# Kernel tuning notes

Hardware: AMD Instinct MI355X
Metric: run time of the kernel (lower is better)

Reference implementation:

```python
import jax, jax.numpy as jnp
import numpy as np

B, N0, D, H = 64, 512, 512, 2048  # graphs, nodes/graph, d_hidden, mlp hidden


def _mlp(x, W1, b1, W2, b2, W3, b3):
    h = jax.nn.relu(x @ W1 + b1)
    h = jax.nn.relu(h @ W2 + b2)
    return h @ W3 + b3


def setup_inputs() -> dict:
    key = jax.random.key(0)
    ks = jax.random.split(key, 16)
    total = B * N0
    x = jax.random.normal(ks[0], (total, D), jnp.float32)
    node_type = jax.random.randint(ks[1], (total,), 0, 4, jnp.int32)
    action_mask = jax.random.bernoulli(ks[2], 0.5, (total,))
    node_indices = jnp.tile(jnp.arange(N0, dtype=jnp.int32), B)
    batch = jnp.repeat(jnp.arange(B, dtype=jnp.int32), N0)
    N = jnp.full((B,), N0, dtype=jnp.int32)

    def lin(k, fan_in, fan_out):
        kw, kb = jax.random.split(k)
        bound = 1.0 / np.sqrt(fan_in)
        W = jax.random.uniform(kw, (fan_in, fan_out), jnp.float32, -bound, bound)
        b = jax.random.uniform(kb, (fan_out,), jnp.float32, -bound, bound)
        return W, b

    mlp_W1, mlp_b1 = lin(ks[3], D, H)
    mlp_W2, mlp_b2 = lin(ks[4], H, H)
    mlp_W3, mlp_b3 = lin(ks[5], H, 1)
    vf_W1, vf_b1 = lin(ks[6], D, H)
    vf_W2, vf_b2 = lin(ks[7], H, H)
    vf_W3, vf_b3 = lin(ks[8], H, 1)
    return dict(x=x, node_type=node_type, action_mask=action_mask,
                node_indices=node_indices, batch=batch, N=N,
                mlp_W1=mlp_W1, mlp_b1=mlp_b1, mlp_W2=mlp_W2, mlp_b2=mlp_b2,
                mlp_W3=mlp_W3, mlp_b3=mlp_b3,
                vf_W1=vf_W1, vf_b1=vf_b1, vf_W2=vf_W2, vf_b2=vf_b2,
                vf_W3=vf_W3, vf_b3=vf_b3)


def reference(x, node_type, action_mask, node_indices, batch, N,
              mlp_W1, mlp_b1, mlp_W2, mlp_b2, mlp_W3, mlp_b3,
              vf_W1, vf_b1, vf_W2, vf_b2, vf_W3, vf_b3):
    nb = N.shape[0]
    # global mean pool over graphs
    counts = jax.ops.segment_sum(jnp.ones((x.shape[0],), x.dtype), batch, num_segments=nb)
    h_mean = jax.ops.segment_sum(x, batch, num_segments=nb) / counts[:, None]
    # masked gather -> MLP -> scatter with -inf fill, expressed as masked select
    z_node = _mlp(x, mlp_W1, mlp_b1, mlp_W2, mlp_b2, mlp_W3, mlp_b3)[:, 0]
    z_all = jnp.where(action_mask, z_node, -jnp.inf)
    z = z_all.reshape(nb, -1)  # multi_length=False: all graphs have N[0] nodes
    v = _mlp(h_mean, vf_W1, vf_b1, vf_W2, vf_b2, vf_W3, vf_b3)
    return z, v
```

## Files before the change

### kernel.cpp

```cpp
#include <hip/hip_runtime.h>
#include <cstdint>
#include <cmath>


typedef __bf16 bf16_t;
typedef float  f32x4  __attribute__((ext_vector_type(4)));
typedef int    i32x4  __attribute__((ext_vector_type(4)));
typedef int    i32x8  __attribute__((ext_vector_type(8)));

#define NB      64
#define N0      512
#define DIM     512
#define HID     2048
#define TOTAL   32768
#define ZNEG    -3.0e38f

__device__ __forceinline__ void gload16(const void* g, void* l) {
  __builtin_amdgcn_global_load_lds(
      (const uint32_t __attribute__((address_space(1)))*)g,
      (uint32_t __attribute__((address_space(3)))*)l, 16, 0, 0);
}

__device__ __forceinline__ unsigned char to_fp8(float f) {
  return (unsigned char)(__builtin_amdgcn_cvt_pk_fp8_f32(f, f, 0, false) & 0xff);
}

__global__ void mask_scan_kernel(const unsigned char* __restrict__ mask,
                                 int* __restrict__ perm,
                                 int* __restrict__ pos,
                                 int* __restrict__ mcount) {
  __shared__ int ts[1024];
  const int t = threadIdx.x;
  const uint32_t* m32 = (const uint32_t*)mask;
  uint32_t w[8];
  int s = 0;
#pragma unroll
  for (int k = 0; k < 8; ++k) {
    w[k] = m32[t * 8 + k];
    s += __popc(w[k] & 0x01010101u);
  }
  ts[t] = s;
  __syncthreads();
  for (int off = 1; off < 1024; off <<= 1) {
    int v = (t >= off) ? ts[t - off] : 0;
    __syncthreads();
    ts[t] += v;
    __syncthreads();
  }
  int run = ts[t] - s;
  const int base = t * 32;
#pragma unroll
  for (int k = 0; k < 32; ++k) {
    int bit = (w[k >> 2] >> ((k & 3) * 8)) & 1;
    if (bit) {
      perm[run] = base + k;
      pos[base + k] = run;
      run++;
    }
  }
  if (t == 1023) {
    mcount[0] = ts[1023];
    mcount[1] = (ts[1023] + 127) & ~127;
  }
}

__global__ void gather_fp8_kernel(const float* __restrict__ x,
                                  const int* __restrict__ perm,
                                  const int* __restrict__ mcount,
                                  uint32_t* __restrict__ xc) {
  const int idx = blockIdx.x * 256 + threadIdx.x;
  const int r = idx >> 7;
  const int c = idx & 127;
  if (r >= mcount[1]) return;
  uint32_t v = 0;
  if (r < mcount[0]) {
    const float4 f = ((const float4*)(x + (size_t)perm[r] * DIM))[c];
    int p = __builtin_amdgcn_cvt_pk_fp8_f32(f.x, f.y, 0, false);
    p = __builtin_amdgcn_cvt_pk_fp8_f32(f.z, f.w, p, true);
    v = (uint32_t)p;
  }
  xc[idx] = v;
}


__global__ void transpose_to_fp8_kernel(const float* __restrict__ W,
                                        uint8_t* __restrict__ Wt,
                                        int K, int N, float scale) {
  __shared__ float tile[32][33];
  const int bx = blockIdx.x;
  const int by = blockIdx.y;
  const int tx = threadIdx.x & 31;
  const int ty = threadIdx.x >> 5;
#pragma unroll
  for (int r = 0; r < 4; ++r)
    tile[ty + r * 8][tx] = W[(size_t)(by * 32 + ty + r * 8) * N + bx * 32 + tx];
  __syncthreads();
#pragma unroll
  for (int r = 0; r < 4; ++r)
    Wt[(size_t)(bx * 32 + ty + r * 8) * K + by * 32 + tx] =
        to_fp8(tile[tx][ty + r * 8] * scale);
}

__global__ void zero_kernel(float* __restrict__ p, int n) {
  int i = blockIdx.x * 256 + threadIdx.x;
  if (i < n) p[i] = 0.f;
}

__global__ void hmean_accum_kernel(const float* __restrict__ x,
                                   float* __restrict__ hsumT) {
  const int g = blockIdx.x >> 3;
  const int slab = blockIdx.x & 7;
  const int c = threadIdx.x;
  const float* xp = x + ((size_t)g * N0 + slab * 64) * DIM + c;
  float s = 0.f;
#pragma unroll 8
  for (int r = 0; r < 64; ++r) s += xp[(size_t)r * DIM];
  atomicAdd(&hsumT[(size_t)c * NB + g], s);
}


__global__ void vf_l1_kernel(const float* __restrict__ hsumT,
                             const float* __restrict__ vW1,
                             const float* __restrict__ vb1,
                             float* __restrict__ vh1t) {
  __shared__ float red[8][32][9];
  const int tx = threadIdx.x & 31;
  const int ty = threadIdx.x >> 5;
  const int n  = blockIdx.x * 32 + tx;
  const int g0 = blockIdx.y * 8;
  float acc[8] = {};
  const float* wp = vW1 + (size_t)(ty * 64) * HID + n;
  const float* hp = hsumT + (size_t)(ty * 64) * NB + g0;
#pragma unroll 4
  for (int kk = 0; kk < 64; ++kk) {
    float w = wp[(size_t)kk * HID];
    float4 h0 = *(const float4*)(hp + kk * NB);
    float4 h1 = *(const float4*)(hp + kk * NB + 4);
    acc[0] += h0.x * w; acc[1] += h0.y * w;
    acc[2] += h0.z * w; acc[3] += h0.w * w;
    acc[4] += h1.x * w; acc[5] += h1.y * w;
    acc[6] += h1.z * w; acc[7] += h1.w * w;
  }
#pragma unroll
  for (int r = 0; r < 8; ++r) red[ty][tx][r] = acc[r];
  __syncthreads();
  if (ty == 0) {
    const float bn = vb1[n];
#pragma unroll
    for (int r = 0; r < 8; ++r) {
      float s = 0.f;
#pragma unroll
      for (int t = 0; t < 8; ++t) s += red[t][tx][r];
      vh1t[(size_t)n * NB + g0 + r] = fmaxf(s * (1.f / 512.f) + bn, 0.f);
    }
  }
}

__global__ void vf_l23_kernel(const float* __restrict__ vh1t,
                              const float* __restrict__ vW2,
                              const float* __restrict__ vb2,
                              const float* __restrict__ vW3,
                              float* __restrict__ vfzp) {
  __shared__ float red[8][32][9];
  const int tx = threadIdx.x & 31;
  const int ty = threadIdx.x >> 5;
  const int n  = blockIdx.x * 32 + tx;
  const int g0 = blockIdx.y * 8;
  float acc[8] = {};
  const float* wp = vW2 + (size_t)(ty * 256) * HID + n;
  const float* hp = vh1t + (size_t)(ty * 256) * NB + g0;
#pragma unroll 4
  for (int kk = 0; kk < 256; ++kk) {
    float w = wp[(size_t)kk * HID];
    float4 h0 = *(const float4*)(hp + kk * NB);
    float4 h1 = *(const float4*)(hp + kk * NB + 4);
    acc[0] += h0.x * w; acc[1] += h0.y * w;
    acc[2] += h0.z * w; acc[3] += h0.w * w;
    acc[4] += h1.x * w; acc[5] += h1.y * w;
    acc[6] += h1.z * w; acc[7] += h1.w * w;
  }
#pragma unroll
  for (int r = 0; r < 8; ++r) red[ty][tx][r] = acc[r];
  __syncthreads();
  if (ty == 0) {
    const float bn = vb2[n];
    const float w3 = vW3[n];
#pragma unroll
    for (int r = 0; r < 8; ++r) {
      float s = 0.f;
#pragma unroll
      for (int t = 0; t < 8; ++t) s += red[t][tx][r];
      float v = fmaxf(s + bn, 0.f) * w3;
#pragma unroll
      for (int off = 16; off; off >>= 1) v += __shfl_down(v, off, 32);
      if (tx == 0) vfzp[(g0 + r) * 64 + blockIdx.x] = v;
    }
  }
}

template <int FUSE>
__global__ __launch_bounds__(256) void gemm_f8(
    const uint8_t* __restrict__ A, const uint8_t* __restrict__ Bt,
    const float* __restrict__ bias, const float* __restrict__ w3,
    uint8_t* __restrict__ C, float* __restrict__ zout,
    const int* __restrict__ mlim, int M, int N, int K, int sb) {
  const int bm = blockIdx.y;
  const int bn = blockIdx.x;
  if (bm * 128 >= *mlim) return;

  __shared__ __align__(16) char Asb[128 * 128];
  __shared__ __align__(16) char Bsb[128 * 128];

  const int tid = threadIdx.x;
  const int wave = tid >> 6;
  const int lane = tid & 63;
  const int lr = lane & 15;
  const int lq = lane >> 4;
  const int swz = lr & 7;
  const int wm = (wave >> 1) << 6;
  const int wn = (wave & 1) << 6;

  const int srow0 = (wave << 3) + (lane >> 3);
  const int gchunk = (lane & 7) ^ (lane >> 3);

  const uint8_t* ag = A + (size_t)(bm * 128 + srow0) * K + (gchunk << 4);
  const uint8_t* bg = Bt + (size_t)(bn * 128 + srow0) * K + (gchunk << 4);
  char* asw = Asb + (wave << 10);
  char* bsw = Bsb + (wave << 10);

  f32x4 acc[4][4] = {};

  for (int k0 = 0; k0 < K; k0 += 128) {
#pragma unroll
    for (int j = 0; j < 4; ++j) {
      gload16(ag + (size_t)(j * 32) * K, asw + j * 4096);
      gload16(bg + (size_t)(j * 32) * K, bsw + j * 4096);
    }
    ag += 128;
    bg += 128;
    __syncthreads();

    i32x8 a8[4], b8[4];
#pragma unroll
    for (int i = 0; i < 4; ++i) {
      const char* base = Asb + ((wm + i * 16 + lr) << 7);
      i32x4 lo = *(const i32x4*)(base + ((((lq << 1) | 0) ^ swz) << 4));
      i32x4 hi = *(const i32x4*)(base + ((((lq << 1) | 1) ^ swz) << 4));
      a8[i] = __builtin_shufflevector(lo, hi, 0, 1, 2, 3, 4, 5, 6, 7);
    }
#pragma unroll
    for (int j = 0; j < 4; ++j) {
      const char* base = Bsb + ((wn + j * 16 + lr) << 7);
      i32x4 lo = *(const i32x4*)(base + ((((lq << 1) | 0) ^ swz) << 4));
      i32x4 hi = *(const i32x4*)(base + ((((lq << 1) | 1) ^ swz) << 4));
      b8[j] = __builtin_shufflevector(lo, hi, 0, 1, 2, 3, 4, 5, 6, 7);
    }
#pragma unroll
    for (int i = 0; i < 4; ++i)
#pragma unroll
      for (int j = 0; j < 4; ++j)
        acc[i][j] = __builtin_amdgcn_mfma_scale_f32_16x16x128_f8f6f4(
            a8[i], b8[j], acc[i][j], 0 , 0 ,
            0, 127 , 0, sb);
    __syncthreads();
  }

  if (FUSE == 0) {
#pragma unroll
    for (int j = 0; j < 4; ++j) {
      const int gc = bn * 128 + wn + j * 16 + lr;
      const float bj = bias[gc];
#pragma unroll
      for (int i = 0; i < 4; ++i) {
        const int gr0 = bm * 128 + wm + i * 16 + lq * 4;
#pragma unroll
        for (int r = 0; r < 4; ++r) {
          float v = fmaxf(acc[i][j][r] + bj, 0.f);
          C[(size_t)(gr0 + r) * N + gc] = to_fp8(v);
        }
      }
    }
  } else {
    float rs[4][4] = {};
#pragma unroll
    for (int j = 0; j < 4; ++j) {
      const int gc = bn * 128 + wn + j * 16 + lr;
      const float bj = bias[gc];
      const float wj = w3[gc];
#pragma unroll
      for (int i = 0; i < 4; ++i)
#pragma unroll
        for (int r = 0; r < 4; ++r)
          rs[i][r] += fmaxf(acc[i][j][r] + bj, 0.f) * wj;
    }
#pragma unroll
    for (int off = 1; off < 16; off <<= 1) {
#pragma unroll
      for (int i = 0; i < 4; ++i)
#pragma unroll
        for (int r = 0; r < 4; ++r)
          rs[i][r] += __shfl_xor(rs[i][r], off, 64);
    }
    if (lr == 0) {
#pragma unroll
      for (int i = 0; i < 4; ++i)
#pragma unroll
        for (int r = 0; r < 4; ++r)
          atomicAdd(&zout[bm * 128 + wm + i * 16 + lq * 4 + r], rs[i][r]);
    }
  }
}

__global__ void finalize_kernel(const float* __restrict__ zp,
                                const float* __restrict__ vfzp,
                                const unsigned char* __restrict__ mask,
                                const int* __restrict__ pos,
                                const float* __restrict__ b3,
                                const float* __restrict__ vb3,
                                float* __restrict__ out) {
  int i = blockIdx.x * 256 + threadIdx.x;
  if (i < TOTAL) {
    out[i] = mask[i] ? (zp[pos[i]] + b3[0]) : ZNEG;
  } else if (i < TOTAL + NB) {
    int g = i - TOTAL;
    float v = 0.f;
#pragma unroll 8
    for (int b = 0; b < 64; ++b) v += vfzp[g * 64 + b];
    out[i] = v + vb3[0];
  }
}

extern "C" void kernel_launch(void* const* d_in, const int* in_sizes, int n_in,
                              void* d_out, int out_size, void* d_ws,
                              size_t ws_size, hipStream_t stream) {
  (void)in_sizes; (void)n_in; (void)out_size; (void)ws_size;
  const float* x    = (const float*)d_in[0];
  const unsigned char* mask = (const unsigned char*)d_in[2];
  const float* W1   = (const float*)d_in[6];
  const float* b1   = (const float*)d_in[7];
  const float* W2   = (const float*)d_in[8];
  const float* b2   = (const float*)d_in[9];
  const float* W3   = (const float*)d_in[10];
  const float* b3   = (const float*)d_in[11];
  const float* vW1  = (const float*)d_in[12];
  const float* vb1  = (const float*)d_in[13];
  const float* vW2  = (const float*)d_in[14];
  const float* vb2  = (const float*)d_in[15];
  const float* vW3  = (const float*)d_in[16];
  const float* vb3  = (const float*)d_in[17];
  float* out = (float*)d_out;

  char* p = (char*)d_ws;
  size_t off = 0;
  auto alloc = [&](size_t bytes) {
    void* r = p + off;
    off = (off + bytes + 255) & ~(size_t)255;
    return r;
  };
  uint8_t* x_f8  = (uint8_t*)alloc((size_t)TOTAL * DIM);
  uint8_t* W1t   = (uint8_t*)alloc((size_t)HID * DIM);
  uint8_t* W2t   = (uint8_t*)alloc((size_t)HID * HID);
  uint8_t* H1    = (uint8_t*)alloc((size_t)TOTAL * HID);
  float*   vh1t  = (float*)alloc((size_t)HID * NB * 4);
  float*   vfzp  = (float*)alloc((size_t)NB * 64 * 4);
  int*     perm  = (int*)alloc((size_t)TOTAL * 4);
  int*     pos   = (int*)alloc((size_t)TOTAL * 4);
  int*     mcount= (int*)alloc(256);
  float*   zreg  = (float*)alloc((size_t)(DIM * NB + TOTAL) * 4);
  float*   hsumT = zreg;
  float*   zpart = zreg + DIM * NB;

  mask_scan_kernel<<<1, 1024, 0, stream>>>(mask, perm, pos, mcount);
  gather_fp8_kernel<<<TOTAL * 128 / 256, 256, 0, stream>>>(
      x, perm, mcount, (uint32_t*)x_f8);

  transpose_to_fp8_kernel<<<dim3(HID / 32, DIM / 32), 256, 0, stream>>>(
      W1, W1t, DIM, HID, 16.f);
  transpose_to_fp8_kernel<<<dim3(HID / 32, HID / 32), 256, 0, stream>>>(
      W2, W2t, HID, HID, 32.f);
  const int nzero = DIM * NB + TOTAL;
  zero_kernel<<<(nzero + 255) / 256, 256, 0, stream>>>(zreg, nzero);

  hmean_accum_kernel<<<NB * 8, 512, 0, stream>>>(x, hsumT);

  vf_l1_kernel<<<dim3(64, 8), 256, 0, stream>>>(hsumT, vW1, vb1, vh1t);
  vf_l23_kernel<<<dim3(64, 8), 256, 0, stream>>>(vh1t, vW2, vb2, vW3, vfzp);

  gemm_f8<0><<<dim3(HID / 128, TOTAL / 128), 256, 0, stream>>>(
      x_f8, W1t, b1, nullptr, H1, nullptr, mcount + 1, TOTAL, HID, DIM, 123);
  gemm_f8<1><<<dim3(HID / 128, TOTAL / 128), 256, 0, stream>>>(
      H1, W2t, b2, W3, nullptr, zpart, mcount + 1, TOTAL, HID, HID, 122);

  finalize_kernel<<<(TOTAL + NB + 255) / 256, 256, 0, stream>>>(
      zpart, vfzp, mask, pos, b3, vb3, out);
}
```

Measured before the change: 281.4 us.

## Split value-head GEMVs along K with partial-sum buffers and finalize kernels

The value-function MLP layers are reworked into a split-K scheme. A generic partial kernel writes per-K-slice partial sums over a grid with 2 or 4 slices, and small finalize kernels add bias and ReLU, and for layer 2 also apply the W3 dot product. This exposes more blocks for the small weight-bound GEMVs. The cost is two extra launches and extra partial-buffer traffic, which may not pay off since the value head is small next to the FP8 GEMMs.

```diff
diff --git a/kernel.cpp b/kernel.cpp
--- a/kernel.cpp
+++ b/kernel.cpp
@@ -118,21 +118,22 @@
   atomicAdd(&hsumT[(size_t)c * NB + g], s);
 }
 
-
-__global__ void vf_l1_kernel(const float* __restrict__ hsumT,
-                             const float* __restrict__ vW1,
-                             const float* __restrict__ vb1,
-                             float* __restrict__ vh1t) {
+__global__ void vf_partial_kernel(const float* __restrict__ h,
+                                  const float* __restrict__ W,
+                                  float* __restrict__ pacc,
+                                  int kspan) {
   __shared__ float red[8][32][9];
   const int tx = threadIdx.x & 31;
   const int ty = threadIdx.x >> 5;
   const int n  = blockIdx.x * 32 + tx;
   const int g0 = blockIdx.y * 8;
+  const int iters = kspan >> 3;
+  const int k0 = blockIdx.z * kspan + ty * iters;
   float acc[8] = {};
-  const float* wp = vW1 + (size_t)(ty * 64) * HID + n;
-  const float* hp = hsumT + (size_t)(ty * 64) * NB + g0;
-#pragma unroll 4
-  for (int kk = 0; kk < 64; ++kk) {
+  const float* wp = W + (size_t)k0 * HID + n;
+  const float* hp = h + (size_t)k0 * NB + g0;
+#pragma unroll 8
+  for (int kk = 0; kk < iters; ++kk) {
     float w = wp[(size_t)kk * HID];
     float4 h0 = *(const float4*)(hp + kk * NB);
     float4 h1 = *(const float4*)(hp + kk * NB + 4);
@@ -145,57 +146,45 @@
   for (int r = 0; r < 8; ++r) red[ty][tx][r] = acc[r];
   __syncthreads();
   if (ty == 0) {
-    const float bn = vb1[n];
 #pragma unroll
     for (int r = 0; r < 8; ++r) {
       float s = 0.f;
 #pragma unroll
       for (int t = 0; t < 8; ++t) s += red[t][tx][r];
-      vh1t[(size_t)n * NB + g0 + r] = fmaxf(s * (1.f / 512.f) + bn, 0.f);
-    }
-  }
-}
-
-__global__ void vf_l23_kernel(const float* __restrict__ vh1t,
-                              const float* __restrict__ vW2,
-                              const float* __restrict__ vb2,
-                              const float* __restrict__ vW3,
-                              float* __restrict__ vfzp) {
-  __shared__ float red[8][32][9];
-  const int tx = threadIdx.x & 31;
-  const int ty = threadIdx.x >> 5;
-  const int n  = blockIdx.x * 32 + tx;
-  const int g0 = blockIdx.y * 8;
-  float acc[8] = {};
-  const float* wp = vW2 + (size_t)(ty * 256) * HID + n;
-  const float* hp = vh1t + (size_t)(ty * 256) * NB + g0;
-#pragma unroll 4
-  for (int kk = 0; kk < 256; ++kk) {
-    float w = wp[(size_t)kk * HID];
-    float4 h0 = *(const float4*)(hp + kk * NB);
-    float4 h1 = *(const float4*)(hp + kk * NB + 4);
-    acc[0] += h0.x * w; acc[1] += h0.y * w;
-    acc[2] += h0.z * w; acc[3] += h0.w * w;
-    acc[4] += h1.x * w; acc[5] += h1.y * w;
-    acc[6] += h1.z * w; acc[7] += h1.w * w;
-  }
-#pragma unroll
-  for (int r = 0; r < 8; ++r) red[ty][tx][r] = acc[r];
+      pacc[((size_t)blockIdx.z * NB + g0 + r) * HID + n] = s;
+    }
+  }
+}
+
+__global__ void vf_l1_fin_kernel(const float* __restrict__ pacc1,
+                                 const float* __restrict__ vb1,
+                                 float* __restrict__ vh1t) {
+  const int idx = blockIdx.x * 256 + threadIdx.x;
+  const int g = idx >> 11;
+  const int n = idx & 2047;
+  float s = pacc1[(size_t)g * HID + n] +
+            pacc1[(size_t)(NB + g) * HID + n];
+  vh1t[(size_t)n * NB + g] = fmaxf(s * (1.f / 512.f) + vb1[n], 0.f);
+}
+
+__global__ void vf_l23_fin_kernel(const float* __restrict__ pacc2,
+                                  const float* __restrict__ vb2,
+                                  const float* __restrict__ vW3,
+                                  float* __restrict__ vfzp) {
+  __shared__ float rs[4];
+  const int g = blockIdx.x >> 3;
+  const int n = (blockIdx.x & 7) * 256 + threadIdx.x;
+  float s = 0.f;
+#pragma unroll
+  for (int kg = 0; kg < 4; ++kg)
+    s += pacc2[((size_t)kg * NB + g) * HID + n];
+  float t = fmaxf(s + vb2[n], 0.f) * vW3[n];
+#pragma unroll
+  for (int off = 32; off; off >>= 1) t += __shfl_down(t, off, 64);
+  if ((threadIdx.x & 63) == 0) rs[threadIdx.x >> 6] = t;
   __syncthreads();
-  if (ty == 0) {
-    const float bn = vb2[n];
-    const float w3 = vW3[n];
-#pragma unroll
-    for (int r = 0; r < 8; ++r) {
-      float s = 0.f;
-#pragma unroll
-      for (int t = 0; t < 8; ++t) s += red[t][tx][r];
-      float v = fmaxf(s + bn, 0.f) * w3;
-#pragma unroll
-      for (int off = 16; off; off >>= 1) v += __shfl_down(v, off, 32);
-      if (tx == 0) vfzp[(g0 + r) * 64 + blockIdx.x] = v;
-    }
-  }
+  if (threadIdx.x == 0)
+    vfzp[g * 8 + (blockIdx.x & 7)] = rs[0] + rs[1] + rs[2] + rs[3];
 }
 
 template <int FUSE>
@@ -324,8 +313,8 @@
   } else if (i < TOTAL + NB) {
     int g = i - TOTAL;
     float v = 0.f;
-#pragma unroll 8
-    for (int b = 0; b < 64; ++b) v += vfzp[g * 64 + b];
+#pragma unroll
+    for (int b = 0; b < 8; ++b) v += vfzp[g * 8 + b];
     out[i] = v + vb3[0];
   }
 }
@@ -362,7 +351,9 @@
   uint8_t* W2t   = (uint8_t*)alloc((size_t)HID * HID);
   uint8_t* H1    = (uint8_t*)alloc((size_t)TOTAL * HID);
   float*   vh1t  = (float*)alloc((size_t)HID * NB * 4);
-  float*   vfzp  = (float*)alloc((size_t)NB * 64 * 4);
+  float*   pacc1 = (float*)alloc((size_t)2 * NB * HID * 4);
+  float*   pacc2 = (float*)alloc((size_t)4 * NB * HID * 4);
+  float*   vfzp  = (float*)alloc((size_t)NB * 8 * 4);
   int*     perm  = (int*)alloc((size_t)TOTAL * 4);
   int*     pos   = (int*)alloc((size_t)TOTAL * 4);
   int*     mcount= (int*)alloc(256);
@@ -383,8 +374,12 @@
 
   hmean_accum_kernel<<<NB * 8, 512, 0, stream>>>(x, hsumT);
 
-  vf_l1_kernel<<<dim3(64, 8), 256, 0, stream>>>(hsumT, vW1, vb1, vh1t);
-  vf_l23_kernel<<<dim3(64, 8), 256, 0, stream>>>(vh1t, vW2, vb2, vW3, vfzp);
+  vf_partial_kernel<<<dim3(64, 8, 2), 256, 0, stream>>>(
+      hsumT, vW1, pacc1, 256);
+  vf_l1_fin_kernel<<<512, 256, 0, stream>>>(pacc1, vb1, vh1t);
+  vf_partial_kernel<<<dim3(64, 8, 4), 256, 0, stream>>>(
+      vh1t, vW2, pacc2, 512);
+  vf_l23_fin_kernel<<<512, 256, 0, stream>>>(pacc2, vb2, vW3, vfzp);
 
   gemm_f8<0><<<dim3(HID / 128, TOTAL / 128), 256, 0, stream>>>(
       x_f8, W1t, b1, nullptr, H1, nullptr, mcount + 1, TOTAL, HID, DIM, 123);
```

New measurement: 283.6 us. Within noise of the previous version (+0.8%).
